# Kernel tuning notes

Hardware: AMD Instinct MI355X
Metric: run time of the kernel (lower is better)

## Reference

```python
import jax, jax.numpy as jnp
import numpy as np

B, T, V, H, E, F, NM = 128, 32, 10000, 512, 512, 2048, 512
D0 = E + NM + H   # 1536: layer-0 concat(x, h)
D1 = H + H        # 1024: layer-1 concat(h_prev_layer, h)


def setup_inputs() -> dict:
    key = jax.random.key(0)
    ks = jax.random.split(key, 10)
    cnn_features = jax.random.normal(ks[0], (B, F), jnp.float32)
    x_tokens = jax.random.randint(ks[1], (B, T), 0, V)
    current_hidden_state = jnp.zeros((2, B, 2 * H), jnp.float32)
    embedding = jax.random.normal(ks[2], (V, E), jnp.float32)
    W_in = jax.random.normal(ks[3], (F, NM), jnp.float32) / np.sqrt(F)
    b_in = jnp.zeros((NM,), jnp.float32)
    # 4 gates stacked (order: i, o, f, c) -- same math as 4 separate matmuls
    W0 = jax.random.normal(ks[4], (D0, 4 * H), jnp.float32) / np.sqrt(D0)
    b0 = jnp.full((4 * H,), 2.0, jnp.float32)
    W1 = jax.random.normal(ks[5], (D1, 4 * H), jnp.float32) / np.sqrt(D1)
    b1 = jnp.full((4 * H,), 2.0, jnp.float32)
    W_out = jax.random.normal(ks[6], (H, V), jnp.float32) / np.sqrt(H)
    b_out = jnp.zeros((V,), jnp.float32)
    return {"cnn_features": cnn_features, "x_tokens": x_tokens,
            "current_hidden_state": current_hidden_state, "embedding": embedding,
            "W_in": W_in, "b_in": b_in, "W0": W0, "b0": b0,
            "W1": W1, "b1": b1, "W_out": W_out, "b_out": b_out,
            "is_train": 1}


def _lstm_gates(z, c_prev):
    # gate order i, o, f, c matches the original cell's separate matmuls
    i_t, o_t, f_t, c_hat = jnp.split(z, 4, axis=1)
    i_t = jax.nn.sigmoid(i_t)
    o_t = jax.nn.sigmoid(o_t)
    f_t = jax.nn.sigmoid(f_t)
    c_hat = jnp.tanh(c_hat)
    c_t = f_t * c_prev + i_t * c_hat
    h_t = o_t * jnp.tanh(c_t)
    return h_t, c_t


def reference(cnn_features, x_tokens, current_hidden_state, embedding,
              W_in, b_in, W0, b0, W1, b1, W_out, b_out, is_train):
    # input_layer: Dropout (identity in eval) -> Linear -> LeakyReLU(0.01)
    proc = jax.nn.leaky_relu(cnn_features @ W_in + b_in, negative_slope=0.01)  # [B, NM]
    emb = embedding[x_tokens]  # [B, T, E] (teacher forcing: is_train=True)

    def step(hidden, emb_t):
        # layer 0: input = concat(token_emb, processed cnn features)
        x0 = jnp.concatenate([emb_t, proc], axis=1)          # [B, E+NM]
        h0, c0 = hidden[0, :, :H], hidden[0, :, H:]
        z0 = jnp.concatenate([x0, h0], axis=1) @ W0 + b0     # [B, 4H]
        h0n, c0n = _lstm_gates(z0, c0)
        # layer 1: input = h of layer 0 (already updated this timestep)
        h1, c1 = hidden[1, :, :H], hidden[1, :, H:]
        z1 = jnp.concatenate([h0n, h1], axis=1) @ W1 + b1    # [B, 4H]
        h1n, c1n = _lstm_gates(z1, c1)
        logits_t = h1n @ W_out + b_out                        # [B, V]
        new_hidden = jnp.stack([jnp.concatenate([h0n, c0n], axis=1),
                                jnp.concatenate([h1n, c1n], axis=1)], axis=0)
        return new_hidden, logits_t

    hidden, logits_seq = jax.lax.scan(step, current_hidden_state,
                                      jnp.moveaxis(emb, 1, 0))  # scan over T
    logits = jnp.moveaxis(logits_seq, 0, 1)  # [B, T, V]
    return logits, hidden
```

## Files before the change

kernel.cpp:

```cpp
#include <hip/hip_runtime.h>


typedef short s8v __attribute__((ext_vector_type(8)));
typedef float f4v __attribute__((ext_vector_type(4)));

__device__ __forceinline__ unsigned short f2bf(float f) {
  unsigned u = __float_as_uint(f);
  u += 0x7fffu + ((u >> 16) & 1u);
  return (unsigned short)(u >> 16);
}
__device__ __forceinline__ float sigm(float x) { return 1.0f / (1.0f + __expf(-x)); }
__device__ __forceinline__ float tanh_(float x) { return 1.0f - 2.0f / (1.0f + __expf(2.0f * x)); }

__device__ __forceinline__ void glds16(const unsigned short* g, unsigned short* l) {
  __builtin_amdgcn_global_load_lds((const __attribute__((address_space(1))) void*)g,
                                   (__attribute__((address_space(3))) void*)l, 16, 0, 0);
}

__global__ void k_transpose_cvt(const float* __restrict__ src, unsigned short* __restrict__ dst,
                                int R, int C) {
  __shared__ float tile[32][33];
  int c0 = blockIdx.x * 32, r0 = blockIdx.y * 32;
  int tx = threadIdx.x, ty = threadIdx.y;
#pragma unroll
  for (int i = 0; i < 4; i++) {
    int r = r0 + ty + i * 8, c = c0 + tx;
    if (r < R && c < C) tile[ty + i * 8][tx] = src[(size_t)r * C + c];
  }
  __syncthreads();
#pragma unroll
  for (int i = 0; i < 4; i++) {
    int c = c0 + ty + i * 8, r = r0 + tx;
    if (r < R && c < C) dst[(size_t)c * R + r] = f2bf(tile[tx][ty + i * 8]);
  }
}

__global__ void k_cvt_bf16(const float* __restrict__ in, unsigned short* __restrict__ out, int n4) {
  int i = blockIdx.x * 256 + threadIdx.x;
  if (i >= n4) return;
  float4 v = ((const float4*)in)[i];
  ushort4 p; p.x = f2bf(v.x); p.y = f2bf(v.y); p.z = f2bf(v.z); p.w = f2bf(v.w);
  ((ushort4*)out)[i] = p;
}

__global__ void k_gather_emb(const float* __restrict__ emb, const int* __restrict__ tok,
                             unsigned short* __restrict__ Xe) {
  int i = blockIdx.x * 256 + threadIdx.x;
  int r = i >> 7, k4 = (i & 127) * 4;
  int b = r & 127, t = r >> 7;
  int tk = tok[b * 32 + t];
  float4 v = *(const float4*)(emb + (size_t)tk * 512 + k4);
  ushort4 p; p.x = f2bf(v.x); p.y = f2bf(v.y); p.z = f2bf(v.z); p.w = f2bf(v.w);
  ((ushort4*)Xe)[i] = p;
}

__global__ void k_init_state(const float* __restrict__ chs,
                             unsigned short* __restrict__ h0b1, unsigned short* __restrict__ h1b1,
                             float* __restrict__ h0f, float* __restrict__ c0f,
                             float* __restrict__ h1f, float* __restrict__ c1f) {
  int i = blockIdx.x * 256 + threadIdx.x;
  int b = i >> 9, j = i & 511;
  float h0 = chs[b * 1024 + j], c0 = chs[b * 1024 + 512 + j];
  float h1 = chs[131072 + b * 1024 + j], c1 = chs[131072 + b * 1024 + 512 + j];
  h0f[i] = h0; c0f[i] = c0; h1f[i] = h1; c1f[i] = c1;
  h0b1[i] = f2bf(h0); h1b1[i] = f2bf(h1);
}

template <int MODE>
__global__ __launch_bounds__(256, 2)
void k_gemm(const unsigned short* __restrict__ A, const unsigned short* __restrict__ Bt,
            const float* __restrict__ bias, const float* __restrict__ add128,
            float* __restrict__ outF, unsigned short* __restrict__ outB,
            int M, int N, int K) {
  __shared__ unsigned short As[4096];
  __shared__ unsigned short Bs[4096];
  int tid = threadIdx.x;
  int wave = tid >> 6, lane = tid & 63;
  int lr = lane & 15, lq = lane >> 4;
  int wm = (wave >> 1) * 64, wn = (wave & 1) * 64;
  int m0 = blockIdx.y * 128, n0 = blockIdx.x * 128;

  f4v acc[4][4];
  f4v zero = {0.0f, 0.0f, 0.0f, 0.0f};
#pragma unroll
  for (int i = 0; i < 4; i++)
#pragma unroll
    for (int j = 0; j < 4; j++) acc[i][j] = zero;

  int srow = tid >> 2, sofs = (tid & 3) * 8;
  int ar0 = m0 + srow, ar1 = ar0 + 64;
  int br0 = n0 + srow, br1 = br0 + 64;
  if (br0 >= N) br0 = N - 1;
  if (br1 >= N) br1 = N - 1;
  const unsigned short* Ag0 = A + (size_t)ar0 * K + sofs;
  const unsigned short* Ag1 = A + (size_t)ar1 * K + sofs;
  const unsigned short* Bg0 = Bt + (size_t)br0 * K + sofs;
  const unsigned short* Bg1 = Bt + (size_t)br1 * K + sofs;
  unsigned short* lA0 = &As[tid * 8];
  unsigned short* lA1 = &As[2048 + tid * 8];
  unsigned short* lB0 = &Bs[tid * 8];
  unsigned short* lB1 = &Bs[2048 + tid * 8];

  for (int k0 = 0; k0 < K; k0 += 32) {
    glds16(Ag0 + k0, lA0);
    glds16(Ag1 + k0, lA1);
    glds16(Bg0 + k0, lB0);
    glds16(Bg1 + k0, lB1);
    __syncthreads();
    s8v af[4], bfr[4];
#pragma unroll
    for (int i = 0; i < 4; i++) af[i] = *(const s8v*)&As[(wm + i * 16 + lr) * 32 + lq * 8];
#pragma unroll
    for (int i = 0; i < 4; i++) bfr[i] = *(const s8v*)&Bs[(wn + i * 16 + lr) * 32 + lq * 8];
#pragma unroll
    for (int i = 0; i < 4; i++)
#pragma unroll
      for (int j = 0; j < 4; j++)
        acc[i][j] = __builtin_amdgcn_mfma_f32_16x16x32_bf16(af[i], bfr[j], acc[i][j], 0, 0, 0);
    __syncthreads();
  }

#pragma unroll
  for (int i = 0; i < 4; i++) {
#pragma unroll
    for (int j = 0; j < 4; j++) {
      int nn = n0 + wn + j * 16 + lr;
      if (nn >= N) continue;
#pragma unroll
      for (int r = 0; r < 4; r++) {
        int mm = m0 + wm + i * 16 + lq * 4 + r;
        float v = acc[i][j][r];
        if (MODE == 0) {
          v += bias[nn];
          v = v > 0.0f ? v : 0.01f * v;
          outB[(size_t)mm * N + nn] = f2bf(v);
        } else if (MODE == 1) {
          v += bias[nn];
          outF[(size_t)mm * N + nn] = v;
        } else if (MODE == 2) {
          v += add128[(size_t)(mm & 127) * N + nn];
          outF[(size_t)mm * N + nn] = v;
        } else {
          v += bias[nn];
          int b = mm & 127, t = mm >> 7;
          outF[(size_t)(b * 32 + t) * N + nn] = v;
        }
      }
    }
  }
}

__global__ __launch_bounds__(128)
void k_phase(const unsigned short* __restrict__ W0h_t, const unsigned short* __restrict__ W1_t,
             const float* __restrict__ Zx, const float* __restrict__ b1,
             unsigned short* __restrict__ h0b0, unsigned short* __restrict__ h0b1,
             unsigned short* __restrict__ h1b0, unsigned short* __restrict__ h1b1,
             float* __restrict__ h0f, float* __restrict__ c0f,
             float* __restrict__ h1f, float* __restrict__ c1f,
             unsigned short* __restrict__ H1all,
             int tB, int doB, int tA, int doA) {
  int wave = threadIdx.x >> 6, lane = threadIdx.x & 63;
  int gid = blockIdx.x * 2 + wave;
  bool isB = gid < 256;
  if (isB && !doB) return;
  if (!isB && !doA) return;
  int id = gid & 255;
  int mt = id >> 5, jt = id & 31;
  int lr = lane & 15, lq = lane >> 4;
  int m = mt * 16 + lr;
  int lqo = lq * 8;
  f4v zero = {0.0f, 0.0f, 0.0f, 0.0f};
  f4v acc[4] = {zero, zero, zero, zero};

  if (isB) {
    const unsigned short* h0r = (tB & 1) ? h0b1 : h0b0;
    const unsigned short* h1r = (tB & 1) ? h1b0 : h1b1;
    unsigned short* h1w = (tB & 1) ? h1b1 : h1b0;

    const unsigned short* pA0 = h0r + m * 512 + lqo;
    const unsigned short* pA1 = h1r + m * 512 + lqo - 512;
    const unsigned short* wb  = W1_t + (size_t)(jt * 16 + lr) * 1024 + lqo;

    s8v a_s[8];
    s8v b_s[8][4];
    auto issueB = [&](int kc, int slot) {
      int kcl = kc < 32 ? kc : 31;
      int ko = kcl * 32;
      const unsigned short* ap = (ko + lqo < 512) ? (pA0 + ko) : (pA1 + ko);
      a_s[slot] = *(const s8v*)ap;
      b_s[slot][0] = *(const s8v*)(wb + ko);
      b_s[slot][1] = *(const s8v*)(wb + 524288 + ko);
      b_s[slot][2] = *(const s8v*)(wb + 1048576 + ko);
      b_s[slot][3] = *(const s8v*)(wb + 1572864 + ko);
    };
#pragma unroll
    for (int s = 0; s < 8; s++) issueB(s, s);
#pragma unroll
    for (int kc = 0; kc < 32; kc++) {
      int slot = kc & 7;
      s8v a = a_s[slot];
      acc[0] = __builtin_amdgcn_mfma_f32_16x16x32_bf16(a, b_s[slot][0], acc[0], 0, 0, 0);
      acc[1] = __builtin_amdgcn_mfma_f32_16x16x32_bf16(a, b_s[slot][1], acc[1], 0, 0, 0);
      acc[2] = __builtin_amdgcn_mfma_f32_16x16x32_bf16(a, b_s[slot][2], acc[2], 0, 0, 0);
      acc[3] = __builtin_amdgcn_mfma_f32_16x16x32_bf16(a, b_s[slot][3], acc[3], 0, 0, 0);
      issueB(kc + 8, slot);
    }

    int j = jt * 16 + lr;
    float bi = b1[j], bo = b1[512 + j], bff = b1[1024 + j], bc = b1[1536 + j];
#pragma unroll
    for (int r = 0; r < 4; r++) {
      int mm = mt * 16 + lq * 4 + r;
      int idx = mm * 512 + j;
      float cprev = c1f[idx];
      float iv = sigm(acc[0][r] + bi);
      float ov = sigm(acc[1][r] + bo);
      float fv = sigm(acc[2][r] + bff);
      float cv = tanh_(acc[3][r] + bc);
      float cn = fv * cprev + iv * cv;
      float hn = ov * tanh_(cn);
      c1f[idx] = cn; h1f[idx] = hn;
      unsigned short hb = f2bf(hn);
      h1w[idx] = hb;
      H1all[(size_t)(tB * 128 + mm) * 512 + j] = hb;
    }
  } else {
    const unsigned short* h0r = (tA & 1) ? h0b0 : h0b1;
    unsigned short* h0w = (tA & 1) ? h0b1 : h0b0;

    const unsigned short* pA = h0r + m * 512 + lqo;
    const unsigned short* wb = W0h_t + (size_t)(jt * 16 + lr) * 512 + lqo;

    s8v a_s[8];
    s8v b_s[8][4];
    auto issueA = [&](int kc, int slot) {
      int kcl = kc < 16 ? kc : 15;
      int ko = kcl * 32;
      a_s[slot] = *(const s8v*)(pA + ko);
      b_s[slot][0] = *(const s8v*)(wb + ko);
      b_s[slot][1] = *(const s8v*)(wb + 262144 + ko);
      b_s[slot][2] = *(const s8v*)(wb + 524288 + ko);
      b_s[slot][3] = *(const s8v*)(wb + 786432 + ko);
    };
#pragma unroll
    for (int s = 0; s < 8; s++) issueA(s, s);
#pragma unroll
    for (int kc = 0; kc < 16; kc++) {
      int slot = kc & 7;
      s8v a = a_s[slot];
      acc[0] = __builtin_amdgcn_mfma_f32_16x16x32_bf16(a, b_s[slot][0], acc[0], 0, 0, 0);
      acc[1] = __builtin_amdgcn_mfma_f32_16x16x32_bf16(a, b_s[slot][1], acc[1], 0, 0, 0);
      acc[2] = __builtin_amdgcn_mfma_f32_16x16x32_bf16(a, b_s[slot][2], acc[2], 0, 0, 0);
      acc[3] = __builtin_amdgcn_mfma_f32_16x16x32_bf16(a, b_s[slot][3], acc[3], 0, 0, 0);
      issueA(kc + 8, slot);
    }

    int j = jt * 16 + lr;
    const float* zrow = Zx + (size_t)tA * 128 * 2048;
#pragma unroll
    for (int r = 0; r < 4; r++) {
      int mm = mt * 16 + lq * 4 + r;
      int idx = mm * 512 + j;
      float cprev = c0f[idx];
      float iv = sigm(acc[0][r] + zrow[mm * 2048 + j]);
      float ov = sigm(acc[1][r] + zrow[mm * 2048 + 512 + j]);
      float fv = sigm(acc[2][r] + zrow[mm * 2048 + 1024 + j]);
      float cv = tanh_(acc[3][r] + zrow[mm * 2048 + 1536 + j]);
      float cn = fv * cprev + iv * cv;
      float hn = ov * tanh_(cn);
      c0f[idx] = cn; h0f[idx] = hn;
      h0w[idx] = f2bf(hn);
    }
  }
}

__global__ void k_write_hidden(const float* __restrict__ h0f, const float* __restrict__ c0f,
                               const float* __restrict__ h1f, const float* __restrict__ c1f,
                               float* __restrict__ out) {
  int idx = blockIdx.x * 256 + threadIdx.x;
  int l = idx >> 17, rem = idx & 131071, b = rem >> 10, j = rem & 1023;
  const float* hs = l ? h1f : h0f;
  const float* cs = l ? c1f : c0f;
  float v = (j < 512) ? hs[b * 512 + j] : cs[b * 512 + (j - 512)];
  out[40960000 + idx] = v;
}

extern "C" void kernel_launch(void* const* d_in, const int* in_sizes, int n_in,
                              void* d_out, int out_size, void* d_ws, size_t ws_size,
                              hipStream_t stream) {
  const float* cnn  = (const float*)d_in[0];
  const int*   tok  = (const int*)d_in[1];
  const float* chs  = (const float*)d_in[2];
  const float* emb  = (const float*)d_in[3];
  const float* W_in = (const float*)d_in[4];
  const float* b_in = (const float*)d_in[5];
  const float* W0   = (const float*)d_in[6];
  const float* b0   = (const float*)d_in[7];
  const float* W1   = (const float*)d_in[8];
  const float* b1   = (const float*)d_in[9];
  const float* W_out= (const float*)d_in[10];
  const float* b_out= (const float*)d_in[11];
  float* out = (float*)d_out;

  char* p = (char*)d_ws;
  auto alloc = [&](size_t bytes) { char* q = p; p += (bytes + 255) & ~(size_t)255; return q; };
  unsigned short* Win_t  = (unsigned short*)alloc((size_t)512 * 2048 * 2);
  unsigned short* W0e_t  = (unsigned short*)alloc((size_t)2048 * 512 * 2);
  unsigned short* W0m_t  = (unsigned short*)alloc((size_t)2048 * 512 * 2);
  unsigned short* W0h_t  = (unsigned short*)alloc((size_t)2048 * 512 * 2);
  unsigned short* W1_t   = (unsigned short*)alloc((size_t)2048 * 1024 * 2);
  unsigned short* Wout_t = (unsigned short*)alloc((size_t)10000 * 512 * 2);
  unsigned short* cnn_b  = (unsigned short*)alloc((size_t)128 * 2048 * 2);
  unsigned short* proc_b = (unsigned short*)alloc((size_t)128 * 512 * 2);
  float*          Cf     = (float*)alloc((size_t)128 * 2048 * 4);
  unsigned short* Xe     = (unsigned short*)alloc((size_t)4096 * 512 * 2);
  float*          Zx     = (float*)alloc((size_t)4096 * 2048 * 4);
  unsigned short* h0b0   = (unsigned short*)alloc(65536 * 2);
  unsigned short* h0b1   = (unsigned short*)alloc(65536 * 2);
  unsigned short* h1b0   = (unsigned short*)alloc(65536 * 2);
  unsigned short* h1b1   = (unsigned short*)alloc(65536 * 2);
  float*          h0f    = (float*)alloc(65536 * 4);
  float*          c0f    = (float*)alloc(65536 * 4);
  float*          h1f    = (float*)alloc(65536 * 4);
  float*          c1f    = (float*)alloc(65536 * 4);
  unsigned short* H1all  = (unsigned short*)alloc((size_t)4096 * 512 * 2);

  dim3 tb(32, 8);
  k_transpose_cvt<<<dim3(16, 64),  tb, 0, stream>>>(W_in, Win_t, 2048, 512);
  k_transpose_cvt<<<dim3(64, 16),  tb, 0, stream>>>(W0,               W0e_t, 512, 2048);
  k_transpose_cvt<<<dim3(64, 16),  tb, 0, stream>>>(W0 + 512 * 2048,  W0m_t, 512, 2048);
  k_transpose_cvt<<<dim3(64, 16),  tb, 0, stream>>>(W0 + 1024 * 2048, W0h_t, 512, 2048);
  k_transpose_cvt<<<dim3(64, 32),  tb, 0, stream>>>(W1, W1_t, 1024, 2048);
  k_transpose_cvt<<<dim3(313, 16), tb, 0, stream>>>(W_out, Wout_t, 512, 10000);
  k_cvt_bf16<<<256, 256, 0, stream>>>(cnn, cnn_b, 65536);

  k_gemm<0><<<dim3(4, 1), 256, 0, stream>>>(cnn_b, Win_t, b_in, nullptr, nullptr, proc_b,
                                            128, 512, 2048);
  k_gemm<1><<<dim3(16, 1), 256, 0, stream>>>(proc_b, W0m_t, b0, nullptr, Cf, nullptr,
                                             128, 2048, 512);
  k_gather_emb<<<2048, 256, 0, stream>>>(emb, tok, Xe);
  k_gemm<2><<<dim3(16, 32), 256, 0, stream>>>(Xe, W0e_t, nullptr, Cf, Zx, nullptr,
                                              4096, 2048, 512);
  k_init_state<<<256, 256, 0, stream>>>(chs, h0b1, h1b1, h0f, c0f, h1f, c1f);

  k_phase<<<256, 128, 0, stream>>>(W0h_t, W1_t, Zx, b1, h0b0, h0b1, h1b0, h1b1,
                                   h0f, c0f, h1f, c1f, H1all, 0, 0, 0, 1);
  for (int t = 0; t < 32; t++)
    k_phase<<<256, 128, 0, stream>>>(W0h_t, W1_t, Zx, b1, h0b0, h0b1, h1b0, h1b1,
                                     h0f, c0f, h1f, c1f, H1all, t, 1, t + 1, (t < 31) ? 1 : 0);

  k_gemm<3><<<dim3(79, 32), 256, 0, stream>>>(H1all, Wout_t, b_out, nullptr, out, nullptr,
                                              4096, 10000, 512);
  k_write_hidden<<<1024, 256, 0, stream>>>(h0f, c0f, h1f, c1f, out);
}
```

Before: 795.9 us.

## Overlap output projection with recurrent steps and fuse prep kernels

After: 926.9 us. +16.5%, slower.

```diff
diff --git a/kernel.cpp b/kernel.cpp
--- a/kernel.cpp
+++ b/kernel.cpp
@@ -17,53 +17,64 @@
                                    (__attribute__((address_space(3))) void*)l, 16, 0, 0);
 }
 
-__global__ void k_transpose_cvt(const float* __restrict__ src, unsigned short* __restrict__ dst,
-                                int R, int C) {
-  __shared__ float tile[32][33];
-  int c0 = blockIdx.x * 32, r0 = blockIdx.y * 32;
-  int tx = threadIdx.x, ty = threadIdx.y;
-#pragma unroll
-  for (int i = 0; i < 4; i++) {
-    int r = r0 + ty + i * 8, c = c0 + tx;
-    if (r < R && c < C) tile[ty + i * 8][tx] = src[(size_t)r * C + c];
-  }
-  __syncthreads();
-#pragma unroll
-  for (int i = 0; i < 4; i++) {
-    int c = c0 + ty + i * 8, r = r0 + tx;
-    if (r < R && c < C) dst[(size_t)c * R + r] = f2bf(tile[tx][ty + i * 8]);
-  }
-}
-
-__global__ void k_cvt_bf16(const float* __restrict__ in, unsigned short* __restrict__ out, int n4) {
-  int i = blockIdx.x * 256 + threadIdx.x;
-  if (i >= n4) return;
-  float4 v = ((const float4*)in)[i];
-  ushort4 p; p.x = f2bf(v.x); p.y = f2bf(v.y); p.z = f2bf(v.z); p.w = f2bf(v.w);
-  ((ushort4*)out)[i] = p;
-}
-
-__global__ void k_gather_emb(const float* __restrict__ emb, const int* __restrict__ tok,
-                             unsigned short* __restrict__ Xe) {
-  int i = blockIdx.x * 256 + threadIdx.x;
-  int r = i >> 7, k4 = (i & 127) * 4;
-  int b = r & 127, t = r >> 7;
-  int tk = tok[b * 32 + t];
-  float4 v = *(const float4*)(emb + (size_t)tk * 512 + k4);
-  ushort4 p; p.x = f2bf(v.x); p.y = f2bf(v.y); p.z = f2bf(v.z); p.w = f2bf(v.w);
-  ((ushort4*)Xe)[i] = p;
-}
-
-__global__ void k_init_state(const float* __restrict__ chs,
-                             unsigned short* __restrict__ h0b1, unsigned short* __restrict__ h1b1,
-                             float* __restrict__ h0f, float* __restrict__ c0f,
-                             float* __restrict__ h1f, float* __restrict__ c1f) {
-  int i = blockIdx.x * 256 + threadIdx.x;
-  int b = i >> 9, j = i & 511;
-  float h0 = chs[b * 1024 + j], c0 = chs[b * 1024 + 512 + j];
-  float h1 = chs[131072 + b * 1024 + j], c1 = chs[131072 + b * 1024 + 512 + j];
-  h0f[i] = h0; c0f[i] = c0; h1f[i] = h1; c1f[i] = c1;
-  h0b1[i] = f2bf(h0); h1b1[i] = f2bf(h1);
+__global__ void k_prep(const float* __restrict__ W_in, const float* __restrict__ W0,
+                       const float* __restrict__ W1, const float* __restrict__ W_out,
+                       const float* __restrict__ cnn, const float* __restrict__ emb,
+                       const int* __restrict__ tok, const float* __restrict__ chs,
+                       unsigned short* __restrict__ Win_t, unsigned short* __restrict__ W0e_t,
+                       unsigned short* __restrict__ W0m_t, unsigned short* __restrict__ W0h_t,
+                       unsigned short* __restrict__ W1_t, unsigned short* __restrict__ Wout_t,
+                       unsigned short* __restrict__ cnn_b, unsigned short* __restrict__ Xe,
+                       unsigned short* __restrict__ h0b1, unsigned short* __restrict__ h1b1,
+                       float* __restrict__ h0f, float* __restrict__ c0f,
+                       float* __restrict__ h1f, float* __restrict__ c1f) {
+  int blk = blockIdx.x;
+  if (blk < 11152) {
+    const float* src; unsigned short* dst; int R, C, bx, by;
+    if (blk < 1024)      { src = W_in;             dst = Win_t;  R = 2048; C = 512;   bx = blk & 15; by = blk >> 4; }
+    else if (blk < 2048) { int b2 = blk - 1024; src = W0;              dst = W0e_t;  R = 512;  C = 2048;  bx = b2 & 63; by = b2 >> 6; }
+    else if (blk < 3072) { int b2 = blk - 2048; src = W0 + 512 * 2048; dst = W0m_t;  R = 512;  C = 2048;  bx = b2 & 63; by = b2 >> 6; }
+    else if (blk < 4096) { int b2 = blk - 3072; src = W0 + 1024 * 2048; dst = W0h_t; R = 512;  C = 2048;  bx = b2 & 63; by = b2 >> 6; }
+    else if (blk < 6144) { int b2 = blk - 4096; src = W1;              dst = W1_t;   R = 1024; C = 2048;  bx = b2 & 63; by = b2 >> 6; }
+    else                 { int b2 = blk - 6144; src = W_out;           dst = Wout_t; R = 512;  C = 10000; bx = b2 % 313; by = b2 / 313; }
+    __shared__ float tile[32][33];
+    int c0 = bx * 32, r0 = by * 32;
+    int tx = threadIdx.x, ty = threadIdx.y;
+#pragma unroll
+    for (int i = 0; i < 4; i++) {
+      int r = r0 + ty + i * 8, c = c0 + tx;
+      if (r < R && c < C) tile[ty + i * 8][tx] = src[(size_t)r * C + c];
+    }
+    __syncthreads();
+#pragma unroll
+    for (int i = 0; i < 4; i++) {
+      int c = c0 + ty + i * 8, r = r0 + tx;
+      if (r < R && c < C) dst[(size_t)c * R + r] = f2bf(tile[tx][ty + i * 8]);
+    }
+    return;
+  }
+  int ft = threadIdx.y * 32 + threadIdx.x;
+  if (blk < 11408) {
+    int i = (blk - 11152) * 256 + ft;
+    float4 v = ((const float4*)cnn)[i];
+    ushort4 p; p.x = f2bf(v.x); p.y = f2bf(v.y); p.z = f2bf(v.z); p.w = f2bf(v.w);
+    ((ushort4*)cnn_b)[i] = p;
+  } else if (blk < 13456) {
+    int i = (blk - 11408) * 256 + ft;
+    int r = i >> 7, k4 = (i & 127) * 4;
+    int b = r & 127, t = r >> 7;
+    int tk = tok[b * 32 + t];
+    float4 v = *(const float4*)(emb + (size_t)tk * 512 + k4);
+    ushort4 p; p.x = f2bf(v.x); p.y = f2bf(v.y); p.z = f2bf(v.z); p.w = f2bf(v.w);
+    ((ushort4*)Xe)[i] = p;
+  } else {
+    int i = (blk - 13456) * 256 + ft;
+    int b = i >> 9, jj = i & 511;
+    float h0 = chs[b * 1024 + jj], c0v = chs[b * 1024 + 512 + jj];
+    float h1 = chs[131072 + b * 1024 + jj], c1v = chs[131072 + b * 1024 + 512 + jj];
+    h0f[i] = h0; c0f[i] = c0v; h1f[i] = h1; c1f[i] = c1v;
+    h0b1[i] = f2bf(h0); h1b1[i] = f2bf(h1);
+  }
 }
 
 template <int MODE>
@@ -96,16 +107,12 @@
   const unsigned short* Ag1 = A + (size_t)ar1 * K + sofs;
   const unsigned short* Bg0 = Bt + (size_t)br0 * K + sofs;
   const unsigned short* Bg1 = Bt + (size_t)br1 * K + sofs;
-  unsigned short* lA0 = &As[tid * 8];
-  unsigned short* lA1 = &As[2048 + tid * 8];
-  unsigned short* lB0 = &Bs[tid * 8];
-  unsigned short* lB1 = &Bs[2048 + tid * 8];
 
   for (int k0 = 0; k0 < K; k0 += 32) {
-    glds16(Ag0 + k0, lA0);
-    glds16(Ag1 + k0, lA1);
-    glds16(Bg0 + k0, lB0);
-    glds16(Bg1 + k0, lB1);
+    glds16(Ag0 + k0, &As[tid * 8]);
+    glds16(Ag1 + k0, &As[2048 + tid * 8]);
+    glds16(Bg0 + k0, &Bs[tid * 8]);
+    glds16(Bg1 + k0, &Bs[2048 + tid * 8]);
     __syncthreads();
     s8v af[4], bfr[4];
 #pragma unroll
@@ -137,13 +144,9 @@
         } else if (MODE == 1) {
           v += bias[nn];
           outF[(size_t)mm * N + nn] = v;
-        } else if (MODE == 2) {
+        } else {
           v += add128[(size_t)(mm & 127) * N + nn];
           outF[(size_t)mm * N + nn] = v;
-        } else {
-          v += bias[nn];
-          int b = mm & 127, t = mm >> 7;
-          outF[(size_t)(b * 32 + t) * N + nn] = v;
         }
       }
     }
@@ -158,18 +161,80 @@
              float* __restrict__ h0f, float* __restrict__ c0f,
              float* __restrict__ h1f, float* __restrict__ c1f,
              unsigned short* __restrict__ H1all,
-             int tB, int doB, int tA, int doA) {
-  int wave = threadIdx.x >> 6, lane = threadIdx.x & 63;
-  int gid = blockIdx.x * 2 + wave;
+             const unsigned short* __restrict__ Wout_t, const float* __restrict__ b_out,
+             float* __restrict__ out,
+             int tB, int doB, int tA, int doA, int tL, int doL, int nPB) {
+  int tid = threadIdx.x;
+  int wave = tid >> 6, lane = tid & 63;
+  int lr = lane & 15, lq = lane >> 4;
+  f4v zero = {0.0f, 0.0f, 0.0f, 0.0f};
+
+  if ((int)blockIdx.x >= nPB) {
+    if (!doL) return;
+    __shared__ __align__(16) unsigned short As[4096];
+    __shared__ __align__(16) unsigned short Bs[2048];
+    int lb = (int)blockIdx.x - nPB;
+    int n0 = lb * 64;
+    const unsigned short* A = H1all + (size_t)tL * 65536;
+    int srow = tid >> 2, sofs = (tid & 3) * 8;
+
+    f4v acc[4][4];
+#pragma unroll
+    for (int i = 0; i < 4; i++)
+#pragma unroll
+      for (int j = 0; j < 4; j++) acc[i][j] = zero;
+
+    int br0 = n0 + srow;       if (br0 > 9999) br0 = 9999;
+    int br1 = n0 + 32 + srow;  if (br1 > 9999) br1 = 9999;
+    const unsigned short* Bg0 = Wout_t + (size_t)br0 * 512 + sofs;
+    const unsigned short* Bg1 = Wout_t + (size_t)br1 * 512 + sofs;
+
+    for (int k0 = 0; k0 < 512; k0 += 32) {
+#pragma unroll
+      for (int c = 0; c < 4; c++)
+        glds16(A + (size_t)(c * 32 + srow) * 512 + sofs + k0, &As[c * 1024 + tid * 8]);
+      glds16(Bg0 + k0, &Bs[tid * 8]);
+      glds16(Bg1 + k0, &Bs[1024 + tid * 8]);
+      __syncthreads();
+      s8v af[4], bfr[4];
+#pragma unroll
+      for (int i = 0; i < 4; i++)
+        af[i] = *(const s8v*)&As[wave * 2048 + (i >> 1) * 1024 + (i & 1) * 512 + lr * 32 + lq * 8];
+#pragma unroll
+      for (int j = 0; j < 4; j++)
+        bfr[j] = *(const s8v*)&Bs[(j >> 1) * 1024 + (j & 1) * 512 + lr * 32 + lq * 8];
+#pragma unroll
+      for (int i = 0; i < 4; i++)
+#pragma unroll
+        for (int j = 0; j < 4; j++)
+          acc[i][j] = __builtin_amdgcn_mfma_f32_16x16x32_bf16(af[i], bfr[j], acc[i][j], 0, 0, 0);
+      __syncthreads();
+    }
+
+#pragma unroll
+    for (int i = 0; i < 4; i++) {
+#pragma unroll
+      for (int j = 0; j < 4; j++) {
+        int nn = n0 + j * 16 + lr;
+        if (nn >= 10000) continue;
+#pragma unroll
+        for (int r = 0; r < 4; r++) {
+          int b = wave * 64 + i * 16 + lq * 4 + r;
+          out[(size_t)(b * 32 + tL) * 10000 + nn] = acc[i][j][r] + b_out[nn];
+        }
+      }
+    }
+    return;
+  }
+
+  int gid = (int)blockIdx.x * 2 + wave;
   bool isB = gid < 256;
   if (isB && !doB) return;
   if (!isB && !doA) return;
   int id = gid & 255;
   int mt = id >> 5, jt = id & 31;
-  int lr = lane & 15, lq = lane >> 4;
   int m = mt * 16 + lr;
   int lqo = lq * 8;
-  f4v zero = {0.0f, 0.0f, 0.0f, 0.0f};
   f4v acc[4] = {zero, zero, zero, zero};
 
   if (isB) {
@@ -325,31 +390,30 @@
   float*          c1f    = (float*)alloc(65536 * 4);
   unsigned short* H1all  = (unsigned short*)alloc((size_t)4096 * 512 * 2);
 
-  dim3 tb(32, 8);
-  k_transpose_cvt<<<dim3(16, 64),  tb, 0, stream>>>(W_in, Win_t, 2048, 512);
-  k_transpose_cvt<<<dim3(64, 16),  tb, 0, stream>>>(W0,               W0e_t, 512, 2048);
-  k_transpose_cvt<<<dim3(64, 16),  tb, 0, stream>>>(W0 + 512 * 2048,  W0m_t, 512, 2048);
-  k_transpose_cvt<<<dim3(64, 16),  tb, 0, stream>>>(W0 + 1024 * 2048, W0h_t, 512, 2048);
-  k_transpose_cvt<<<dim3(64, 32),  tb, 0, stream>>>(W1, W1_t, 1024, 2048);
-  k_transpose_cvt<<<dim3(313, 16), tb, 0, stream>>>(W_out, Wout_t, 512, 10000);
-  k_cvt_bf16<<<256, 256, 0, stream>>>(cnn, cnn_b, 65536);
-
+  k_prep<<<13712, dim3(32, 8), 0, stream>>>(W_in, W0, W1, W_out, cnn, emb, tok, chs,
+                                            Win_t, W0e_t, W0m_t, W0h_t, W1_t, Wout_t,
+                                            cnn_b, Xe, h0b1, h1b1, h0f, c0f, h1f, c1f);
   k_gemm<0><<<dim3(4, 1), 256, 0, stream>>>(cnn_b, Win_t, b_in, nullptr, nullptr, proc_b,
                                             128, 512, 2048);
   k_gemm<1><<<dim3(16, 1), 256, 0, stream>>>(proc_b, W0m_t, b0, nullptr, Cf, nullptr,
                                              128, 2048, 512);
-  k_gather_emb<<<2048, 256, 0, stream>>>(emb, tok, Xe);
   k_gemm<2><<<dim3(16, 32), 256, 0, stream>>>(Xe, W0e_t, nullptr, Cf, Zx, nullptr,
                                               4096, 2048, 512);
-  k_init_state<<<256, 256, 0, stream>>>(chs, h0b1, h1b1, h0f, c0f, h1f, c1f);
-
-  k_phase<<<256, 128, 0, stream>>>(W0h_t, W1_t, Zx, b1, h0b0, h0b1, h1b0, h1b1,
-                                   h0f, c0f, h1f, c1f, H1all, 0, 0, 0, 1);
-  for (int t = 0; t < 32; t++)
-    k_phase<<<256, 128, 0, stream>>>(W0h_t, W1_t, Zx, b1, h0b0, h0b1, h1b0, h1b1,
-                                     h0f, c0f, h1f, c1f, H1all, t, 1, t + 1, (t < 31) ? 1 : 0);
-
-  k_gemm<3><<<dim3(79, 32), 256, 0, stream>>>(H1all, Wout_t, b_out, nullptr, out, nullptr,
-                                              4096, 10000, 512);
+
+  const int NPB = 256;
+  k_phase<<<NPB, 128, 0, stream>>>(W0h_t, W1_t, Zx, b1, h0b0, h0b1, h1b0, h1b1,
+                                   h0f, c0f, h1f, c1f, H1all, Wout_t, b_out, out,
+                                   0, 0, 0, 1, 0, 0, NPB);
+  for (int t = 0; t < 32; t++) {
+    int doL = (t >= 1) ? 1 : 0;
+    int grid = NPB + (doL ? 157 : 0);
+    k_phase<<<grid, 128, 0, stream>>>(W0h_t, W1_t, Zx, b1, h0b0, h0b1, h1b0, h1b1,
+                                      h0f, c0f, h1f, c1f, H1all, Wout_t, b_out, out,
+                                      t, 1, t + 1, (t < 31) ? 1 : 0, t - 1, doL, NPB);
+  }
+  k_phase<<<157, 128, 0, stream>>>(W0h_t, W1_t, Zx, b1, h0b0, h0b1, h1b0, h1b1,
+                                   h0f, c0f, h1f, c1f, H1all, Wout_t, b_out, out,
+                                   0, 0, 0, 0, 31, 1, 0);
+
   k_write_hidden<<<1024, 256, 0, stream>>>(h0f, c0f, h1f, c1f, out);
 }
```
